# Performance work log

Hardware: AMD Instinct MI355X
Metric: run time of the kernel (lower is better)

## Reference

```python
import jax, jax.numpy as jnp
import numpy as np

N_NODES = 100000
N_EDGES = 600000
N_GRAPHS = 256
K = 5
N_FEAT = 16
N_CLASSES = 4


def setup_inputs() -> dict:
    key = jax.random.key(0)
    ks = jax.random.split(key, 12)
    x = jax.random.normal(ks[0], (N_NODES, N_FEAT), dtype=jnp.float32)
    edge_index = jax.random.randint(ks[1], (2, N_EDGES), 0, N_NODES, dtype=jnp.int32)
    batch = jnp.sort(jax.random.randint(ks[2], (N_NODES,), 0, N_GRAPHS, dtype=jnp.int32))
    s = 0.1
    W11 = jax.random.normal(ks[3], (K, N_FEAT, 64), dtype=jnp.float32) * s
    b11 = jnp.zeros((64,), dtype=jnp.float32)
    W12 = jax.random.normal(ks[4], (K, N_FEAT, 64), dtype=jnp.float32) * s
    b12 = jnp.zeros((64,), dtype=jnp.float32)
    W21 = jax.random.normal(ks[5], (K, 128, 256), dtype=jnp.float32) * s
    b21 = jnp.zeros((256,), dtype=jnp.float32)
    W22 = jax.random.normal(ks[6], (K, 128, 256), dtype=jnp.float32) * s
    b22 = jnp.zeros((256,), dtype=jnp.float32)
    fc_w = jax.random.normal(ks[7], (512, N_CLASSES), dtype=jnp.float32) * s
    fc_b = jnp.zeros((N_CLASSES,), dtype=jnp.float32)
    return {
        "x": x, "edge_index": edge_index, "batch": batch,
        "W11": W11, "b11": b11, "W12": W12, "b12": b12,
        "W21": W21, "b21": b21, "W22": W22, "b22": b22,
        "fc_w": fc_w, "fc_b": fc_b,
    }


def _cheb_norm(src, dst, n_nodes):
    # PyG ChebConv (sym norm, lambda_max=2): L_hat = -D^{-1/2} A D^{-1/2},
    # zero diagonal. Degree computed over source (row) indices.
    deg = jax.ops.segment_sum(jnp.ones_like(src, dtype=jnp.float32), src,
                              num_segments=n_nodes)
    dinv = jnp.where(deg > 0, jax.lax.rsqrt(jnp.maximum(deg, 1.0)), 0.0)
    return -dinv[src] * dinv[dst]


def _cheb_conv(x, src, dst, w_norm, W, b):
    # Chebyshev recursion: Tx0=x, Tx1=L_hat x, Txk = 2 L_hat Tx_{k-1} - Tx_{k-2}
    n = x.shape[0]

    def spmm(h):  # aggregate messages from src at dst
        return jax.ops.segment_sum(h[src] * w_norm[:, None], dst, num_segments=n)

    Tx0 = x
    Tx1 = spmm(x)
    out = jnp.einsum('nf,fo->no', Tx0, W[0]) + jnp.einsum('nf,fo->no', Tx1, W[1])
    for k in range(2, W.shape[0]):
        Tx2 = 2.0 * spmm(Tx1) - Tx0
        out = out + jnp.einsum('nf,fo->no', Tx2, W[k])
        Tx0, Tx1 = Tx1, Tx2
    return out + b


def reference(x, edge_index, batch, W11, b11, W12, b12, W21, b21, W22, b22,
              fc_w, fc_b):
    src, dst = edge_index[0], edge_index[1]
    w_fwd = _cheb_norm(src, dst, N_NODES)
    w_rev = _cheb_norm(dst, src, N_NODES)  # reversed adjacency

    x1 = jax.nn.relu(_cheb_conv(x, src, dst, w_fwd, W11, b11))
    x2 = jax.nn.relu(_cheb_conv(x, dst, src, w_rev, W12, b12))
    h = jnp.concatenate([x1, x2], axis=1)  # [N, 128]

    x1 = jax.nn.relu(_cheb_conv(h, src, dst, w_fwd, W21, b21))
    x2 = jax.nn.relu(_cheb_conv(h, dst, src, w_rev, W22, b22))
    h = jnp.concatenate([x1, x2], axis=1)  # [N, 512]

    # global mean pool over graphs
    sums = jax.ops.segment_sum(h, batch, num_segments=N_GRAPHS)
    cnt = jax.ops.segment_sum(jnp.ones((h.shape[0],), dtype=h.dtype), batch,
                              num_segments=N_GRAPHS)
    pooled = sums / jnp.maximum(cnt, 1.0)[:, None]  # [G, 512]

    logits = pooled @ fc_w + fc_b
    return jax.nn.log_softmax(logits, axis=1)
```

## Files before the change

### kernel.cpp

```cpp
#include <hip/hip_runtime.h>
#include <stdint.h>

#define NNODES 100000
#define NEDGES 600000
#define NGRAPH 256
#define KCH 5
#define F1 16
#define O1 64
#define F2 128
#define O2 256
#define FT1 (KCH * F1)
#define FT2 (KCH * F2)
#define KSTEPS 20
#define KS1 3
#define NBK 10
#define LROW2 72
#define NXCD 8

typedef unsigned short ushort_t;
typedef __attribute__((ext_vector_type(8))) short bf16x8;
typedef __attribute__((ext_vector_type(4))) float f32x4;

__device__ __forceinline__ float bflo(unsigned int u) {
    union { unsigned int u; float f; } v; v.u = u << 16; return v.f;
}
__device__ __forceinline__ float bfhi(unsigned int u) {
    union { unsigned int u; float f; } v; v.u = u & 0xFFFF0000u; return v.f;
}
__device__ __forceinline__ unsigned int f2bf(float f) {
    union { float f; unsigned int u; } v; v.f = f;
    return (v.u + 0x7FFFu + ((v.u >> 16) & 1u)) >> 16;
}
__device__ __forceinline__ unsigned int pack2(float lo, float hi) {
    return (f2bf(hi) << 16) | f2bf(lo);
}


__global__ void k_count(const int* __restrict__ src, const int* __restrict__ dst,
                        int* __restrict__ cntDst, int* __restrict__ cntSrc, int E) {
    int e = blockIdx.x * 256 + threadIdx.x;
    if (e < E) {
        atomicAdd(&cntDst[dst[e]], 1);
        atomicAdd(&cntSrc[src[e]], 1);
    }
}

__global__ void k_dinv(const int* __restrict__ cntDst, const int* __restrict__ cntSrc,
                       float* __restrict__ dinvF, float* __restrict__ dinvR, int n) {
    int i = blockIdx.x * 256 + threadIdx.x;
    if (i < n) {
        int cs = cntSrc[i], cd = cntDst[i];
        dinvF[i] = cs > 0 ? rsqrtf((float)cs) : 0.f;
        dinvR[i] = cd > 0 ? rsqrtf((float)cd) : 0.f;
    }
}

__global__ void k_scan1(const int* __restrict__ in, int* __restrict__ out,
                        int* __restrict__ blksum, int n) {
    __shared__ int a[512];
    __shared__ int s[256];
    int t = threadIdx.x;
    int base = blockIdx.x * 512;
    a[t]       = (base + t < n)       ? in[base + t]       : 0;
    a[t + 256] = (base + t + 256 < n) ? in[base + t + 256] : 0;
    __syncthreads();
    s[t] = a[2 * t] + a[2 * t + 1];
    __syncthreads();
    for (int off = 1; off < 256; off <<= 1) {
        int v = (t >= off) ? s[t - off] : 0;
        __syncthreads();
        s[t] += v;
        __syncthreads();
    }
    int ep = (t > 0) ? s[t - 1] : 0;
    if (base + 2 * t < n)     out[base + 2 * t]     = ep;
    if (base + 2 * t + 1 < n) out[base + 2 * t + 1] = ep + a[2 * t];
    if (t == 255) blksum[blockIdx.x] = s[255];
}

__global__ void k_scan2(int* __restrict__ blksum, int nb) {
    __shared__ int s[256];
    int t = threadIdx.x;
    s[t] = (t < nb) ? blksum[t] : 0;
    __syncthreads();
    for (int off = 1; off < 256; off <<= 1) {
        int v = (t >= off) ? s[t - off] : 0;
        __syncthreads();
        s[t] += v;
        __syncthreads();
    }
    if (t < nb) blksum[t] = (t > 0) ? s[t - 1] : 0;
}

__global__ void k_scan3(int* __restrict__ out, int* __restrict__ cur,
                        const int* __restrict__ blksum, int n) {
    int i = blockIdx.x * 512 + threadIdx.x;
    int add = blksum[blockIdx.x];
    if (i < n)       { int v = out[i] + add;       out[i] = v;       cur[i] = v; }
    if (i + 256 < n) { int v = out[i + 256] + add; out[i + 256] = v; cur[i + 256] = v; }
}

__global__ void k_tail(int* __restrict__ off_f, int* __restrict__ off_r, int n, int E) {
    if (threadIdx.x == 0) { off_f[n] = E; off_r[n] = E; }
}

__global__ void k_scatter(const int* __restrict__ src, const int* __restrict__ dst,
                          const float* __restrict__ dinvF, const float* __restrict__ dinvR,
                          int* __restrict__ curF, int* __restrict__ curR,
                          int2* __restrict__ edF, int2* __restrict__ edR, int E,
                          int chunk) {
    int c = blockIdx.x & (NXCD - 1);
    int sb = blockIdx.x >> 3;
    int slices = gridDim.x >> 3;
    int lo = c * chunk, hi = lo + chunk;
    for (int e = sb * 256 + threadIdx.x; e < E; e += slices * 256) {
        int s = src[e], d = dst[e];
        if (d >= lo && d < hi) {
            int p = atomicAdd(&curF[d], 1);
            float wf = -dinvF[s] * dinvF[d];
            edF[p] = make_int2(s, __float_as_int(wf));
        }
        if (s >= lo && s < hi) {
            int q = atomicAdd(&curR[s], 1);
            float wr = -dinvR[s] * dinvR[d];
            edR[q] = make_int2(d, __float_as_int(wr));
        }
    }
}

__global__ void k_gstart(const int* __restrict__ batch, int* __restrict__ gstart, int n) {
    int g = blockIdx.x * 64 + threadIdx.x;
    if (g > NGRAPH) return;
    if (g == NGRAPH) { gstart[g] = n; return; }
    int lo = 0, hi = n;
    while (lo < hi) {
        int mid = (lo + hi) >> 1;
        if (batch[mid] < g) lo = mid + 1; else hi = mid;
    }
    gstart[g] = lo;
}


__global__ void k_copyx(const float* __restrict__ x, float* __restrict__ Tx,
                        ushort_t* __restrict__ TxB, int n) {
    int tid = blockIdx.x * 256 + threadIdx.x;
    int r = tid >> 2, c = tid & 3;
    if (r < n) {
        float4 v = *(const float4*)(x + (size_t)r * 16 + c * 4);
        *(float4*)(Tx + (size_t)r * FT1 + c * 4) = v;
        uint2 b;
        b.x = pack2(v.x, v.y);
        b.y = pack2(v.z, v.w);
        *(uint2*)(TxB + (size_t)r * F1 + c * 4) = b;
    }
}

__global__ void k_spmm_f32(const ushort_t* __restrict__ HinB, float* __restrict__ Hout,
                           ushort_t* __restrict__ HoutB,
                           const float* __restrict__ Tx0,
                           const int* __restrict__ off, const int2* __restrict__ ed,
                           int n) {
    int tid = blockIdx.x * 256 + threadIdx.x;
    int r = tid >> 2, c = tid & 3;
    if (r >= n) return;
    int j0 = off[r], j1 = off[r + 1];
    float4 s = {0.f, 0.f, 0.f, 0.f};
    int j = j0;
    for (; j + 4 <= j1; j += 4) {
        int2 e0 = ed[j], e1 = ed[j + 1], e2 = ed[j + 2], e3 = ed[j + 3];
        float wa = __int_as_float(e0.y), wb = __int_as_float(e1.y);
        float wc = __int_as_float(e2.y), wd = __int_as_float(e3.y);
        const uint2 h0 = *(const uint2*)(HinB + (size_t)e0.x * F1 + c * 4);
        const uint2 h1 = *(const uint2*)(HinB + (size_t)e1.x * F1 + c * 4);
        const uint2 h2 = *(const uint2*)(HinB + (size_t)e2.x * F1 + c * 4);
        const uint2 h3 = *(const uint2*)(HinB + (size_t)e3.x * F1 + c * 4);
        s.x = fmaf(wa, bflo(h0.x), s.x); s.y = fmaf(wa, bfhi(h0.x), s.y);
        s.z = fmaf(wa, bflo(h0.y), s.z); s.w = fmaf(wa, bfhi(h0.y), s.w);
        s.x = fmaf(wb, bflo(h1.x), s.x); s.y = fmaf(wb, bfhi(h1.x), s.y);
        s.z = fmaf(wb, bflo(h1.y), s.z); s.w = fmaf(wb, bfhi(h1.y), s.w);
        s.x = fmaf(wc, bflo(h2.x), s.x); s.y = fmaf(wc, bfhi(h2.x), s.y);
        s.z = fmaf(wc, bflo(h2.y), s.z); s.w = fmaf(wc, bfhi(h2.y), s.w);
        s.x = fmaf(wd, bflo(h3.x), s.x); s.y = fmaf(wd, bfhi(h3.x), s.y);
        s.z = fmaf(wd, bflo(h3.y), s.z); s.w = fmaf(wd, bfhi(h3.y), s.w);
    }
    for (; j < j1; ++j) {
        int2 e = ed[j];
        float w2 = __int_as_float(e.y);
        const uint2 h = *(const uint2*)(HinB + (size_t)e.x * F1 + c * 4);
        s.x = fmaf(w2, bflo(h.x), s.x); s.y = fmaf(w2, bfhi(h.x), s.y);
        s.z = fmaf(w2, bflo(h.y), s.z); s.w = fmaf(w2, bfhi(h.y), s.w);
    }
    float4 o;
    if (Tx0) {
        const float4 t0 = *(const float4*)(Tx0 + (size_t)r * FT1 + c * 4);
        o.x = 2.f * s.x - t0.x; o.y = 2.f * s.y - t0.y;
        o.z = 2.f * s.z - t0.z; o.w = 2.f * s.w - t0.w;
    } else {
        o = s;
    }
    *(float4*)(Hout + (size_t)r * FT1 + c * 4) = o;
    uint2 b;
    b.x = pack2(o.x, o.y);
    b.y = pack2(o.z, o.w);
    *(uint2*)(HoutB + (size_t)r * F1 + c * 4) = b;
}

__global__ void k_spmm_bf(const ushort_t* __restrict__ Hin, ushort_t* __restrict__ Hout,
                          const ushort_t* __restrict__ Tx0,
                          const int* __restrict__ off, const int2* __restrict__ ed,
                          int n) {
    int r = blockIdx.x * 4 + (threadIdx.x >> 6);
    r = __builtin_amdgcn_readfirstlane(r);
    int c = threadIdx.x & 63;
    if (r >= n) return;
    int j0 = __builtin_amdgcn_readfirstlane(off[r]);
    int j1 = __builtin_amdgcn_readfirstlane(off[r + 1]);
    float s0 = 0.f, s1 = 0.f;
    int j = j0;
    int jfull = j0 + ((j1 - j0) & ~7);
    for (; j < jfull; j += 8) {
        float w[8];
        unsigned int h[8];
#pragma unroll
        for (int sl = 0; sl < 8; ++sl) {
            int2 e = ed[j + sl];
            w[sl] = __int_as_float(e.y);
            h[sl] = *(const unsigned int*)(Hin + (size_t)e.x * FT2 + c * 2);
        }
#pragma unroll
        for (int sl = 0; sl < 8; ++sl) {
            s0 = fmaf(bflo(h[sl]), w[sl], s0);
            s1 = fmaf(bfhi(h[sl]), w[sl], s1);
        }
    }
    int rem = j1 - j;
    if (rem) {
        float w[8];
        unsigned int h[8];
#pragma unroll
        for (int sl = 0; sl < 8; ++sl) {
            w[sl] = 0.f; h[sl] = 0u;
            if (sl < rem) {
                int2 e = ed[j + sl];
                w[sl] = __int_as_float(e.y);
                h[sl] = *(const unsigned int*)(Hin + (size_t)e.x * FT2 + c * 2);
            }
        }
#pragma unroll
        for (int sl = 0; sl < 8; ++sl) {
            s0 = fmaf(bflo(h[sl]), w[sl], s0);
            s1 = fmaf(bfhi(h[sl]), w[sl], s1);
        }
    }
    if (Tx0) {
        unsigned int t0 = *(const unsigned int*)(Tx0 + (size_t)r * FT2 + c * 2);
        s0 = 2.f * s0 - bflo(t0);
        s1 = 2.f * s1 - bfhi(t0);
    }
    *(unsigned int*)(Hout + (size_t)r * FT2 + c * 2) = pack2(s0, s1);
}

__global__ void k_packW1(const float* __restrict__ W, ushort_t* __restrict__ Bp) {
    int tid = blockIdx.x * 256 + threadIdx.x;
    if (tid >= 4 * KS1 * 64) return;
    int lane = tid & 63;
    int ks = (tid >> 6) % KS1;
    int nt = tid / (64 * KS1);
    int k0 = ks * 32 + (lane >> 4) * 8;
    int ncol = nt * 16 + (lane & 15);
    float v[8];
#pragma unroll
    for (int j = 0; j < 8; ++j) {
        int k = k0 + j;
        v[j] = (k < FT1) ? W[(size_t)k * O1 + ncol] : 0.f;
    }
    uint4 o;
    o.x = pack2(v[0], v[1]); o.y = pack2(v[2], v[3]);
    o.z = pack2(v[4], v[5]); o.w = pack2(v[6], v[7]);
    *(uint4*)(Bp + (size_t)tid * 8) = o;
}

__global__ __launch_bounds__(256) void k_gemm1_mfma(
    const float* __restrict__ A, const ushort_t* __restrict__ Bp,
    const float* __restrict__ bias, ushort_t* __restrict__ out, int n) {
    int lane = threadIdx.x & 63;
    int wvi = threadIdx.x >> 6;
    int mrow = lane & 15;
    int quad = lane >> 4;
    int m0w = blockIdx.x * 64 + wvi * 16;
    int row = m0w + mrow;
    int rowc = row < n ? row : n - 1;
    const float* Ar = A + (size_t)rowc * FT1 + quad * 8;

    f32x4 acc[4] = {};
#pragma unroll
    for (int ks = 0; ks < KS1; ++ks) {
        float4 a0 = *(const float4*)(Ar + ks * 32);
        float4 a1 = *(const float4*)(Ar + ks * 32 + 4);
        union { bf16x8 v; unsigned int u[4]; } ua;
        ua.u[0] = pack2(a0.x, a0.y);
        ua.u[1] = pack2(a0.z, a0.w);
        ua.u[2] = pack2(a1.x, a1.y);
        ua.u[3] = pack2(a1.z, a1.w);
#pragma unroll
        for (int nf = 0; nf < 4; ++nf) {
            bf16x8 bfr = *(const bf16x8*)(Bp + ((size_t)(nf * KS1 + ks) * 64 + lane) * 8);
            acc[nf] = __builtin_amdgcn_mfma_f32_16x16x32_bf16(ua.v, bfr, acc[nf], 0, 0, 0);
        }
    }
#pragma unroll
    for (int nf = 0; nf < 4; ++nf) {
        float bb = bias[nf * 16 + mrow];
#pragma unroll
        for (int reg = 0; reg < 4; ++reg) {
            int orow = m0w + quad * 4 + reg;
            if (orow < n)
                out[(size_t)orow * FT2 + nf * 16 + mrow] =
                    (ushort_t)f2bf(fmaxf(acc[nf][reg] + bb, 0.f));
        }
    }
}

__global__ void k_packW(const float* __restrict__ W, ushort_t* __restrict__ Bp) {
    int tid = blockIdx.x * 256 + threadIdx.x;
    if (tid >= 16 * KSTEPS * 64) return;
    int lane = tid & 63;
    int ks = (tid >> 6) % KSTEPS;
    int nt = tid / (64 * KSTEPS);
    int k0 = ks * 32 + (lane >> 4) * 8;
    int ncol = nt * 16 + (lane & 15);
    float v[8];
#pragma unroll
    for (int j = 0; j < 8; ++j) v[j] = W[(size_t)(k0 + j) * O2 + ncol];
    uint4 o;
    o.x = pack2(v[0], v[1]); o.y = pack2(v[2], v[3]);
    o.z = pack2(v[4], v[5]); o.w = pack2(v[6], v[7]);
    *(uint4*)(Bp + (size_t)tid * 8) = o;
}

__global__ __launch_bounds__(512) void k_gemm2_mfma(
    const ushort_t* __restrict__ A, const ushort_t* __restrict__ Bp,
    const float* __restrict__ bias, float* __restrict__ pooled, int colofs,
    const int* __restrict__ batch, int n) {
    __shared__ ushort_t lds[2][128 * LROW2];

    int lane = threadIdx.x & 63;
    int wv = threadIdx.x >> 6;
    int mhalf = wv >> 2;
    int nquad = wv & 3;
    int m0 = blockIdx.x * 128;
    int mrow = lane & 15;
    int quad = lane >> 4;
    int srow = threadIdx.x >> 2;
    int sc = threadIdx.x & 3;

    const ushort_t* Ag = A + (size_t)(m0 + srow) * FT2 + sc * 8;
    const ushort_t* Bbase = Bp + ((size_t)(nquad * 4) * KSTEPS * 64 + lane) * 8;
    int sidx = srow * LROW2 + sc * 8;
    int rbase = (mhalf * 64) * LROW2;

    f32x4 acc[4][4] = {};
    uint4 nxt0, nxt1;
    bf16x8 bcur[4], bnxt[4];

    *(uint4*)&lds[0][sidx]      = *(const uint4*)(Ag);
    *(uint4*)&lds[0][sidx + 32] = *(const uint4*)(Ag + 32);
    nxt0 = *(const uint4*)(Ag + 64);
    nxt1 = *(const uint4*)(Ag + 96);
#pragma unroll
    for (int nf = 0; nf < 4; ++nf)
        bcur[nf] = *(const bf16x8*)(Bbase + ((size_t)nf * KSTEPS) * 512);

    for (int bk = 0; bk < NBK; ++bk) {
        __syncthreads();
        if (bk + 1 < NBK) {
            *(uint4*)&lds[(bk + 1) & 1][sidx]      = nxt0;
            *(uint4*)&lds[(bk + 1) & 1][sidx + 32] = nxt1;
        }
        if (bk + 2 < NBK) {
            nxt0 = *(const uint4*)(Ag + (bk + 2) * 64);
            nxt1 = *(const uint4*)(Ag + (bk + 2) * 64 + 32);
        }
        const ushort_t* lbuf = &lds[bk & 1][0];
#pragma unroll
        for (int sub = 0; sub < 2; ++sub) {
            int ks = bk * 2 + sub;
            if (ks + 1 < KSTEPS) {
#pragma unroll
                for (int nf = 0; nf < 4; ++nf)
                    bnxt[nf] = *(const bf16x8*)(Bbase + ((size_t)nf * KSTEPS + ks + 1) * 512);
            }
            bf16x8 af[4];
#pragma unroll
            for (int mf = 0; mf < 4; ++mf)
                af[mf] = *(const bf16x8*)(lbuf + rbase + (mf * 16 + mrow) * LROW2 +
                                          sub * 32 + quad * 8);
#pragma unroll
            for (int mf = 0; mf < 4; ++mf)
#pragma unroll
                for (int nf = 0; nf < 4; ++nf)
                    acc[mf][nf] = __builtin_amdgcn_mfma_f32_16x16x32_bf16(
                        af[mf], bcur[nf], acc[mf][nf], 0, 0, 0);
#pragma unroll
            for (int nf = 0; nf < 4; ++nf) bcur[nf] = bnxt[nf];
        }
    }

    float bcol[4];
#pragma unroll
    for (int nf = 0; nf < 4; ++nf) bcol[nf] = bias[nquad * 64 + nf * 16 + mrow];

#pragma unroll
    for (int mf = 0; mf < 4; ++mf) {
        int t0 = m0 + mhalf * 64 + mf * 16;
        if (t0 >= n) break;
        int te = (t0 + 15 < n) ? t0 + 15 : n - 1;
        int r0 = t0 + quad * 4;
        if (batch[t0] == batch[te]) {
            int g = batch[t0];
#pragma unroll
            for (int nf = 0; nf < 4; ++nf) {
                float s = 0.f;
#pragma unroll
                for (int reg = 0; reg < 4; ++reg) {
                    float v = fmaxf(acc[mf][nf][reg] + bcol[nf], 0.f);
                    if (r0 + reg < n) s += v;
                }
                s += __shfl_xor(s, 16, 64);
                s += __shfl_xor(s, 32, 64);
                if (quad == 0)
                    atomicAdd(pooled + (size_t)g * 512 + colofs + nquad * 64 + nf * 16 + mrow, s);
            }
        } else {
            int gb[4];
#pragma unroll
            for (int reg = 0; reg < 4; ++reg)
                gb[reg] = batch[(r0 + reg < n) ? r0 + reg : n - 1];
#pragma unroll
            for (int nf = 0; nf < 4; ++nf) {
                int col = colofs + nquad * 64 + nf * 16 + mrow;
                float run = 0.f;
                int g = gb[0];
                bool any = false;
#pragma unroll
                for (int reg = 0; reg < 4; ++reg) {
                    int row = r0 + reg;
                    if (row >= n) break;
                    float v = fmaxf(acc[mf][nf][reg] + bcol[nf], 0.f);
                    if (gb[reg] != g) {
                        atomicAdd(pooled + (size_t)g * 512 + col, run);
                        run = 0.f;
                        g = gb[reg];
                    }
                    run += v;
                    any = true;
                }
                if (any) atomicAdd(pooled + (size_t)g * 512 + col, run);
            }
        }
    }
}

__global__ void k_logits(const float* __restrict__ pooled, const int* __restrict__ gstart,
                         const float* __restrict__ fcw, const float* __restrict__ fcb,
                         float* __restrict__ out) {
    int g = threadIdx.x;
    int cnt = gstart[g + 1] - gstart[g];
    float inv = 1.f / (float)(cnt > 1 ? cnt : 1);
    float lg[4];
#pragma unroll
    for (int o = 0; o < 4; ++o) lg[o] = fcb[o];
    for (int f = 0; f < 512; ++f) {
        float p = pooled[g * 512 + f] * inv;
#pragma unroll
        for (int o = 0; o < 4; ++o) lg[o] = fmaf(p, fcw[f * 4 + o], lg[o]);
    }
    float m = fmaxf(fmaxf(lg[0], lg[1]), fmaxf(lg[2], lg[3]));
    float s = 0.f;
#pragma unroll
    for (int o = 0; o < 4; ++o) s += expf(lg[o] - m);
    float l = logf(s);
#pragma unroll
    for (int o = 0; o < 4; ++o) out[g * 4 + o] = lg[o] - m - l;
}


extern "C" void kernel_launch(void* const* d_in, const int* in_sizes, int n_in,
                              void* d_out, int out_size, void* d_ws, size_t ws_size,
                              hipStream_t stream) {
    const float* x   = (const float*)d_in[0];
    const int* ei    = (const int*)d_in[1];
    const int* batch = (const int*)d_in[2];
    const float* W11 = (const float*)d_in[3];
    const float* b11 = (const float*)d_in[4];
    const float* W12 = (const float*)d_in[5];
    const float* b12 = (const float*)d_in[6];
    const float* W21 = (const float*)d_in[7];
    const float* b21 = (const float*)d_in[8];
    const float* W22 = (const float*)d_in[9];
    const float* b22 = (const float*)d_in[10];
    const float* fcw = (const float*)d_in[11];
    const float* fcb = (const float*)d_in[12];
    float* out = (float*)d_out;

    const int N = in_sizes[0] / F1;
    const int E = in_sizes[1] / 2;
    const int* src = ei;
    const int* dst = ei + E;

    char* w = (char*)d_ws;
    size_t pos = 0;
    auto alloc = [&](size_t bytes) -> void* {
        void* p = w + pos;
        pos += (bytes + 255) & ~(size_t)255;
        return p;
    };
    int* cur_f   = (int*)alloc((size_t)N * 4);
    int* cur_r   = (int*)alloc((size_t)N * 4);
    int* off_f   = (int*)alloc((size_t)(N + 1) * 4);
    int* off_r   = (int*)alloc((size_t)(N + 1) * 4);
    float* dinvF = (float*)alloc((size_t)N * 4);
    float* dinvR = (float*)alloc((size_t)N * 4);
    int2* ed_f   = (int2*)alloc((size_t)E * 8);
    int2* ed_r   = (int2*)alloc((size_t)E * 8);
    int* blks_f  = (int*)alloc(1024);
    int* blks_r  = (int*)alloc(1024);
    int* gstart  = (int*)alloc((NGRAPH + 1) * 4);
    float* pooled = (float*)alloc((size_t)NGRAPH * 512 * 4);
    ushort_t* BpF = (ushort_t*)alloc((size_t)FT2 * O2 * 2);
    ushort_t* BpR = (ushort_t*)alloc((size_t)FT2 * O2 * 2);
    ushort_t* Bp1F = (ushort_t*)alloc((size_t)4 * KS1 * 64 * 8 * 2);
    ushort_t* Bp1R = (ushort_t*)alloc((size_t)4 * KS1 * 64 * 8 * 2);
    float* TxAll1 = (float*)alloc(((size_t)N * FT1 + 256) * 4);
    ushort_t* TxB1 = (ushort_t*)alloc((size_t)KCH * N * F1 * 2);
    ushort_t* TxAll2 = (ushort_t*)alloc((size_t)(N + 128) * FT2 * 2);

    (void)hipMemsetAsync(cur_f, 0, (size_t)N * 4, stream);
    (void)hipMemsetAsync(cur_r, 0, (size_t)N * 4, stream);
    (void)hipMemsetAsync(pooled, 0, (size_t)NGRAPH * 512 * 4, stream);

    int gE = (E + 255) / 256, gN = (N + 255) / 256;
    k_count<<<gE, 256, 0, stream>>>(src, dst, cur_f, cur_r, E);
    k_dinv<<<gN, 256, 0, stream>>>(cur_f, cur_r, dinvF, dinvR, N);

    int NB = (N + 511) / 512;
    k_scan1<<<NB, 256, 0, stream>>>(cur_f, off_f, blks_f, N);
    k_scan1<<<NB, 256, 0, stream>>>(cur_r, off_r, blks_r, N);
    k_scan2<<<1, 256, 0, stream>>>(blks_f, NB);
    k_scan2<<<1, 256, 0, stream>>>(blks_r, NB);
    k_scan3<<<NB, 256, 0, stream>>>(off_f, cur_f, blks_f, N);
    k_scan3<<<NB, 256, 0, stream>>>(off_r, cur_r, blks_r, N);
    k_tail<<<1, 64, 0, stream>>>(off_f, off_r, N, E);
    int chunk = (N + NXCD - 1) / NXCD;
    k_scatter<<<NXCD * 256, 256, 0, stream>>>(src, dst, dinvF, dinvR, cur_f, cur_r,
                                              ed_f, ed_r, E, chunk);
    k_gstart<<<5, 64, 0, stream>>>(batch, gstart, N);
    k_packW<<<80, 256, 0, stream>>>(W21, BpF);
    k_packW<<<80, 256, 0, stream>>>(W22, BpR);
    k_packW1<<<3, 256, 0, stream>>>(W11, Bp1F);
    k_packW1<<<3, 256, 0, stream>>>(W12, Bp1R);

    k_copyx<<<(N * 4 + 255) / 256, 256, 0, stream>>>(x, TxAll1, TxB1, N);
    int gs1 = (N * 4 + 255) / 256;
    int gg1 = (N + 63) / 64;
    auto C1 = [&](int k) { return TxAll1 + k * F1; };
    auto B1 = [&](int k) { return TxB1 + (size_t)k * N * F1; };
    k_spmm_f32<<<gs1, 256, 0, stream>>>(B1(0), C1(1), B1(1), nullptr, off_f, ed_f, N);
    k_spmm_f32<<<gs1, 256, 0, stream>>>(B1(1), C1(2), B1(2), C1(0), off_f, ed_f, N);
    k_spmm_f32<<<gs1, 256, 0, stream>>>(B1(2), C1(3), B1(3), C1(1), off_f, ed_f, N);
    k_spmm_f32<<<gs1, 256, 0, stream>>>(B1(3), C1(4), B1(4), C1(2), off_f, ed_f, N);
    k_gemm1_mfma<<<gg1, 256, 0, stream>>>(TxAll1, Bp1F, b11, TxAll2, N);
    k_spmm_f32<<<gs1, 256, 0, stream>>>(B1(0), C1(1), B1(1), nullptr, off_r, ed_r, N);
    k_spmm_f32<<<gs1, 256, 0, stream>>>(B1(1), C1(2), B1(2), C1(0), off_r, ed_r, N);
    k_spmm_f32<<<gs1, 256, 0, stream>>>(B1(2), C1(3), B1(3), C1(1), off_r, ed_r, N);
    k_spmm_f32<<<gs1, 256, 0, stream>>>(B1(3), C1(4), B1(4), C1(2), off_r, ed_r, N);
    k_gemm1_mfma<<<gg1, 256, 0, stream>>>(TxAll1, Bp1R, b12, TxAll2 + O1, N);

    int gs2 = (N + 3) / 4;
    auto C2 = [&](int k) { return TxAll2 + k * F2; };
    int gg = (N + 127) / 128;
    k_spmm_bf<<<gs2, 256, 0, stream>>>(C2(0), C2(1), nullptr, off_f, ed_f, N);
    k_spmm_bf<<<gs2, 256, 0, stream>>>(C2(1), C2(2), C2(0), off_f, ed_f, N);
    k_spmm_bf<<<gs2, 256, 0, stream>>>(C2(2), C2(3), C2(1), off_f, ed_f, N);
    k_spmm_bf<<<gs2, 256, 0, stream>>>(C2(3), C2(4), C2(2), off_f, ed_f, N);
    k_gemm2_mfma<<<gg, 512, 0, stream>>>(TxAll2, BpF, b21, pooled, 0, batch, N);
    k_spmm_bf<<<gs2, 256, 0, stream>>>(C2(0), C2(1), nullptr, off_r, ed_r, N);
    k_spmm_bf<<<gs2, 256, 0, stream>>>(C2(1), C2(2), C2(0), off_r, ed_r, N);
    k_spmm_bf<<<gs2, 256, 0, stream>>>(C2(2), C2(3), C2(1), off_r, ed_r, N);
    k_spmm_bf<<<gs2, 256, 0, stream>>>(C2(3), C2(4), C2(2), off_r, ed_r, N);
    k_gemm2_mfma<<<gg, 512, 0, stream>>>(TxAll2, BpR, b22, pooled, 256, batch, N);

    k_logits<<<1, 256, 0, stream>>>(pooled, gstart, fcw, fcb, out);
}
```

Baseline: 794.2 us.

## Merge setup kernels, software-pipeline bf16 SpMM, retile layer-2 GEMM to 4 waves

Several independent changes land together. The forward and reverse scan and weight-pack kernels are merged into single launches, and the tail write is folded into the scan, which cuts launch count. The last layer-1 SpMM step no longer writes an unused bf16 copy. The bf16 SpMM gets a two-block double-buffered gather so that loads of the next 8 edges overlap the FMAs on the current ones. The layer-2 MFMA GEMM moves from 8 waves with 64-wide K blocks to 4 waves with 128 rows per wave and 32-wide K steps, which raises per-wave register use and relies on launch_bounds(256,2) for occupancy.

```diff
diff --git a/kernel.cpp b/kernel.cpp
--- a/kernel.cpp
+++ b/kernel.cpp
@@ -13,8 +13,7 @@
 #define FT2 (KCH * F2)
 #define KSTEPS 20
 #define KS1 3
-#define NBK 10
-#define LROW2 72
+#define LROW 40
 #define NXCD 8
 
 typedef unsigned short ushort_t;
@@ -55,12 +54,18 @@
     }
 }
 
-__global__ void k_scan1(const int* __restrict__ in, int* __restrict__ out,
-                        int* __restrict__ blksum, int n) {
+__global__ void k_scan1m(const int* __restrict__ inF, int* __restrict__ outF,
+                         int* __restrict__ bsF,
+                         const int* __restrict__ inR, int* __restrict__ outR,
+                         int* __restrict__ bsR, int n, int NB) {
     __shared__ int a[512];
     __shared__ int s[256];
+    int b = blockIdx.x;
+    const int* in; int* out; int* bs; int lb;
+    if (b < NB) { in = inF; out = outF; bs = bsF; lb = b; }
+    else        { in = inR; out = outR; bs = bsR; lb = b - NB; }
     int t = threadIdx.x;
-    int base = blockIdx.x * 512;
+    int base = lb * 512;
     a[t]       = (base + t < n)       ? in[base + t]       : 0;
     a[t + 256] = (base + t + 256 < n) ? in[base + t + 256] : 0;
     __syncthreads();
@@ -75,13 +80,14 @@
     int ep = (t > 0) ? s[t - 1] : 0;
     if (base + 2 * t < n)     out[base + 2 * t]     = ep;
     if (base + 2 * t + 1 < n) out[base + 2 * t + 1] = ep + a[2 * t];
-    if (t == 255) blksum[blockIdx.x] = s[255];
-}
-
-__global__ void k_scan2(int* __restrict__ blksum, int nb) {
+    if (t == 255) bs[lb] = s[255];
+}
+
+__global__ void k_scan2m(int* __restrict__ bsF, int* __restrict__ bsR, int nb) {
     __shared__ int s[256];
+    int* bs = (blockIdx.x == 0) ? bsF : bsR;
     int t = threadIdx.x;
-    s[t] = (t < nb) ? blksum[t] : 0;
+    s[t] = (t < nb) ? bs[t] : 0;
     __syncthreads();
     for (int off = 1; off < 256; off <<= 1) {
         int v = (t >= off) ? s[t - off] : 0;
@@ -89,19 +95,22 @@
         s[t] += v;
         __syncthreads();
     }
-    if (t < nb) blksum[t] = (t > 0) ? s[t - 1] : 0;
-}
-
-__global__ void k_scan3(int* __restrict__ out, int* __restrict__ cur,
-                        const int* __restrict__ blksum, int n) {
-    int i = blockIdx.x * 512 + threadIdx.x;
-    int add = blksum[blockIdx.x];
+    if (t < nb) bs[t] = (t > 0) ? s[t - 1] : 0;
+}
+
+__global__ void k_scan3m(int* __restrict__ outF, int* __restrict__ curF,
+                         const int* __restrict__ bsF,
+                         int* __restrict__ outR, int* __restrict__ curR,
+                         const int* __restrict__ bsR, int n, int E, int NB) {
+    int b = blockIdx.x;
+    int* out; int* cur; const int* bs; int lb;
+    if (b < NB) { out = outF; cur = curF; bs = bsF; lb = b; }
+    else        { out = outR; cur = curR; bs = bsR; lb = b - NB; }
+    int i = lb * 512 + threadIdx.x;
+    int add = bs[lb];
     if (i < n)       { int v = out[i] + add;       out[i] = v;       cur[i] = v; }
     if (i + 256 < n) { int v = out[i + 256] + add; out[i + 256] = v; cur[i + 256] = v; }
-}
-
-__global__ void k_tail(int* __restrict__ off_f, int* __restrict__ off_r, int n, int E) {
-    if (threadIdx.x == 0) { off_f[n] = E; off_r[n] = E; }
+    if (lb == 0 && threadIdx.x == 0) out[n] = E;
 }
 
 __global__ void k_scatter(const int* __restrict__ src, const int* __restrict__ dst,
@@ -199,10 +208,12 @@
         o = s;
     }
     *(float4*)(Hout + (size_t)r * FT1 + c * 4) = o;
-    uint2 b;
-    b.x = pack2(o.x, o.y);
-    b.y = pack2(o.z, o.w);
-    *(uint2*)(HoutB + (size_t)r * F1 + c * 4) = b;
+    if (HoutB) {
+        uint2 b;
+        b.x = pack2(o.x, o.y);
+        b.y = pack2(o.z, o.w);
+        *(uint2*)(HoutB + (size_t)r * F1 + c * 4) = b;
+    }
 }
 
 __global__ void k_spmm_bf(const ushort_t* __restrict__ Hin, ushort_t* __restrict__ Hout,
@@ -216,40 +227,47 @@
     int j0 = __builtin_amdgcn_readfirstlane(off[r]);
     int j1 = __builtin_amdgcn_readfirstlane(off[r + 1]);
     float s0 = 0.f, s1 = 0.f;
-    int j = j0;
-    int jfull = j0 + ((j1 - j0) & ~7);
-    for (; j < jfull; j += 8) {
-        float w[8];
-        unsigned int h[8];
+
+    auto loadblk = [&](int jb, float* W, unsigned int* H) {
+        if (jb + 8 <= j1) {
+#pragma unroll
+            for (int sl = 0; sl < 8; ++sl) {
+                int2 e = ed[jb + sl];
+                W[sl] = __int_as_float(e.y);
+                H[sl] = *(const unsigned int*)(Hin + (size_t)e.x * FT2 + c * 2);
+            }
+        } else {
+#pragma unroll
+            for (int sl = 0; sl < 8; ++sl) {
+                W[sl] = 0.f; H[sl] = 0u;
+                if (jb + sl < j1) {
+                    int2 e = ed[jb + sl];
+                    W[sl] = __int_as_float(e.y);
+                    H[sl] = *(const unsigned int*)(Hin + (size_t)e.x * FT2 + c * 2);
+                }
+            }
+        }
+    };
+    auto fmablk = [&](const float* W, const unsigned int* H) {
 #pragma unroll
         for (int sl = 0; sl < 8; ++sl) {
-            int2 e = ed[j + sl];
-            w[sl] = __int_as_float(e.y);
-            h[sl] = *(const unsigned int*)(Hin + (size_t)e.x * FT2 + c * 2);
-        }
-#pragma unroll
-        for (int sl = 0; sl < 8; ++sl) {
-            s0 = fmaf(bflo(h[sl]), w[sl], s0);
-            s1 = fmaf(bfhi(h[sl]), w[sl], s1);
-        }
-    }
-    int rem = j1 - j;
-    if (rem) {
-        float w[8];
-        unsigned int h[8];
-#pragma unroll
-        for (int sl = 0; sl < 8; ++sl) {
-            w[sl] = 0.f; h[sl] = 0u;
-            if (sl < rem) {
-                int2 e = ed[j + sl];
-                w[sl] = __int_as_float(e.y);
-                h[sl] = *(const unsigned int*)(Hin + (size_t)e.x * FT2 + c * 2);
+            s0 = fmaf(bflo(H[sl]), W[sl], s0);
+            s1 = fmaf(bfhi(H[sl]), W[sl], s1);
+        }
+    };
+
+    float wA[8], wB[8];
+    unsigned int hA[8], hB[8];
+    if (j0 < j1) {
+        loadblk(j0, wA, hA);
+        for (int j = j0; j < j1; j += 16) {
+            bool hasB = (j + 8 < j1);
+            if (hasB) loadblk(j + 8, wB, hB);
+            fmablk(wA, hA);
+            if (hasB) {
+                if (j + 16 < j1) loadblk(j + 16, wA, hA);
+                fmablk(wB, hB);
             }
-        }
-#pragma unroll
-        for (int sl = 0; sl < 8; ++sl) {
-            s0 = fmaf(bflo(h[sl]), w[sl], s0);
-            s1 = fmaf(bfhi(h[sl]), w[sl], s1);
         }
     }
     if (Tx0) {
@@ -260,8 +278,12 @@
     *(unsigned int*)(Hout + (size_t)r * FT2 + c * 2) = pack2(s0, s1);
 }
 
-__global__ void k_packW1(const float* __restrict__ W, ushort_t* __restrict__ Bp) {
-    int tid = blockIdx.x * 256 + threadIdx.x;
+__global__ void k_packW1m(const float* __restrict__ WF, ushort_t* __restrict__ BpF_,
+                          const float* __restrict__ WR, ushort_t* __restrict__ BpR_) {
+    int b = blockIdx.x;
+    const float* W = (b < 3) ? WF : WR;
+    ushort_t* Bp = (b < 3) ? BpF_ : BpR_;
+    int tid = ((b < 3) ? b : b - 3) * 256 + threadIdx.x;
     if (tid >= 4 * KS1 * 64) return;
     int lane = tid & 63;
     int ks = (tid >> 6) % KS1;
@@ -321,8 +343,12 @@
     }
 }
 
-__global__ void k_packW(const float* __restrict__ W, ushort_t* __restrict__ Bp) {
-    int tid = blockIdx.x * 256 + threadIdx.x;
+__global__ void k_packWm(const float* __restrict__ WF, ushort_t* __restrict__ BpF_,
+                         const float* __restrict__ WR, ushort_t* __restrict__ BpR_) {
+    int b = blockIdx.x;
+    const float* W = (b < 80) ? WF : WR;
+    ushort_t* Bp = (b < 80) ? BpF_ : BpR_;
+    int tid = ((b < 80) ? b : b - 80) * 256 + threadIdx.x;
     if (tid >= 16 * KSTEPS * 64) return;
     int lane = tid & 63;
     int ks = (tid >> 6) % KSTEPS;
@@ -338,81 +364,73 @@
     *(uint4*)(Bp + (size_t)tid * 8) = o;
 }
 
-__global__ __launch_bounds__(512) void k_gemm2_mfma(
+__global__ __launch_bounds__(256, 2) void k_gemm2_mfma(
     const ushort_t* __restrict__ A, const ushort_t* __restrict__ Bp,
     const float* __restrict__ bias, float* __restrict__ pooled, int colofs,
     const int* __restrict__ batch, int n) {
-    __shared__ ushort_t lds[2][128 * LROW2];
+    __shared__ ushort_t lds[2][128 * LROW];
 
     int lane = threadIdx.x & 63;
     int wv = threadIdx.x >> 6;
-    int mhalf = wv >> 2;
-    int nquad = wv & 3;
     int m0 = blockIdx.x * 128;
     int mrow = lane & 15;
     int quad = lane >> 4;
-    int srow = threadIdx.x >> 2;
-    int sc = threadIdx.x & 3;
-
-    const ushort_t* Ag = A + (size_t)(m0 + srow) * FT2 + sc * 8;
-    const ushort_t* Bbase = Bp + ((size_t)(nquad * 4) * KSTEPS * 64 + lane) * 8;
-    int sidx = srow * LROW2 + sc * 8;
-    int rbase = (mhalf * 64) * LROW2;
-
-    f32x4 acc[4][4] = {};
+    int srow = threadIdx.x >> 1;
+    int sc = threadIdx.x & 1;
+
+    const ushort_t* Ag = A + (size_t)(m0 + srow) * FT2 + sc * 16;
+    const ushort_t* Bbase = Bp + ((size_t)(wv * 4) * KSTEPS * 64 + lane) * 8;
+    int sidx = srow * LROW + sc * 16;
+
+    f32x4 acc[8][4] = {};
     uint4 nxt0, nxt1;
     bf16x8 bcur[4], bnxt[4];
 
-    *(uint4*)&lds[0][sidx]      = *(const uint4*)(Ag);
-    *(uint4*)&lds[0][sidx + 32] = *(const uint4*)(Ag + 32);
-    nxt0 = *(const uint4*)(Ag + 64);
-    nxt1 = *(const uint4*)(Ag + 96);
+    *(uint4*)&lds[0][sidx]     = *(const uint4*)(Ag);
+    *(uint4*)&lds[0][sidx + 8] = *(const uint4*)(Ag + 8);
+    nxt0 = *(const uint4*)(Ag + 32);
+    nxt1 = *(const uint4*)(Ag + 40);
 #pragma unroll
     for (int nf = 0; nf < 4; ++nf)
         bcur[nf] = *(const bf16x8*)(Bbase + ((size_t)nf * KSTEPS) * 512);
 
-    for (int bk = 0; bk < NBK; ++bk) {
+    for (int ks = 0; ks < KSTEPS; ++ks) {
         __syncthreads();
-        if (bk + 1 < NBK) {
-            *(uint4*)&lds[(bk + 1) & 1][sidx]      = nxt0;
-            *(uint4*)&lds[(bk + 1) & 1][sidx + 32] = nxt1;
-        }
-        if (bk + 2 < NBK) {
-            nxt0 = *(const uint4*)(Ag + (bk + 2) * 64);
-            nxt1 = *(const uint4*)(Ag + (bk + 2) * 64 + 32);
-        }
-        const ushort_t* lbuf = &lds[bk & 1][0];
-#pragma unroll
-        for (int sub = 0; sub < 2; ++sub) {
-            int ks = bk * 2 + sub;
-            if (ks + 1 < KSTEPS) {
-#pragma unroll
-                for (int nf = 0; nf < 4; ++nf)
-                    bnxt[nf] = *(const bf16x8*)(Bbase + ((size_t)nf * KSTEPS + ks + 1) * 512);
-            }
-            bf16x8 af[4];
-#pragma unroll
-            for (int mf = 0; mf < 4; ++mf)
-                af[mf] = *(const bf16x8*)(lbuf + rbase + (mf * 16 + mrow) * LROW2 +
-                                          sub * 32 + quad * 8);
-#pragma unroll
-            for (int mf = 0; mf < 4; ++mf)
-#pragma unroll
-                for (int nf = 0; nf < 4; ++nf)
-                    acc[mf][nf] = __builtin_amdgcn_mfma_f32_16x16x32_bf16(
-                        af[mf], bcur[nf], acc[mf][nf], 0, 0, 0);
-#pragma unroll
-            for (int nf = 0; nf < 4; ++nf) bcur[nf] = bnxt[nf];
-        }
+        if (ks + 1 < KSTEPS) {
+            *(uint4*)&lds[(ks + 1) & 1][sidx]     = nxt0;
+            *(uint4*)&lds[(ks + 1) & 1][sidx + 8] = nxt1;
+        }
+        if (ks + 2 < KSTEPS) {
+            nxt0 = *(const uint4*)(Ag + (ks + 2) * 32);
+            nxt1 = *(const uint4*)(Ag + (ks + 2) * 32 + 8);
+        }
+        if (ks + 1 < KSTEPS) {
+#pragma unroll
+            for (int nf = 0; nf < 4; ++nf)
+                bnxt[nf] = *(const bf16x8*)(Bbase + ((size_t)nf * KSTEPS + ks + 1) * 512);
+        }
+        const ushort_t* lbuf = &lds[ks & 1][0];
+        bf16x8 af[8];
+#pragma unroll
+        for (int mf = 0; mf < 8; ++mf)
+            af[mf] = *(const bf16x8*)(lbuf + (mf * 16 + mrow) * LROW + quad * 8);
+#pragma unroll
+        for (int mf = 0; mf < 8; ++mf)
+#pragma unroll
+            for (int nf = 0; nf < 4; ++nf)
+                acc[mf][nf] = __builtin_amdgcn_mfma_f32_16x16x32_bf16(
+                    af[mf], bcur[nf], acc[mf][nf], 0, 0, 0);
+#pragma unroll
+        for (int nf = 0; nf < 4; ++nf) bcur[nf] = bnxt[nf];
     }
 
     float bcol[4];
 #pragma unroll
-    for (int nf = 0; nf < 4; ++nf) bcol[nf] = bias[nquad * 64 + nf * 16 + mrow];
-
-#pragma unroll
-    for (int mf = 0; mf < 4; ++mf) {
-        int t0 = m0 + mhalf * 64 + mf * 16;
+    for (int nf = 0; nf < 4; ++nf) bcol[nf] = bias[wv * 64 + nf * 16 + mrow];
+
+#pragma unroll
+    for (int mf = 0; mf < 8; ++mf) {
+        int t0 = m0 + mf * 16;
         if (t0 >= n) break;
         int te = (t0 + 15 < n) ? t0 + 15 : n - 1;
         int r0 = t0 + quad * 4;
@@ -429,7 +447,7 @@
                 s += __shfl_xor(s, 16, 64);
                 s += __shfl_xor(s, 32, 64);
                 if (quad == 0)
-                    atomicAdd(pooled + (size_t)g * 512 + colofs + nquad * 64 + nf * 16 + mrow, s);
+                    atomicAdd(pooled + (size_t)g * 512 + colofs + wv * 64 + nf * 16 + mrow, s);
             }
         } else {
             int gb[4];
@@ -438,7 +456,7 @@
                 gb[reg] = batch[(r0 + reg < n) ? r0 + reg : n - 1];
 #pragma unroll
             for (int nf = 0; nf < 4; ++nf) {
-                int col = colofs + nquad * 64 + nf * 16 + mrow;
+                int col = colofs + wv * 64 + nf * 16 + mrow;
                 float run = 0.f;
                 int g = gb[0];
                 bool any = false;
@@ -544,21 +562,15 @@
     k_dinv<<<gN, 256, 0, stream>>>(cur_f, cur_r, dinvF, dinvR, N);
 
     int NB = (N + 511) / 512;
-    k_scan1<<<NB, 256, 0, stream>>>(cur_f, off_f, blks_f, N);
-    k_scan1<<<NB, 256, 0, stream>>>(cur_r, off_r, blks_r, N);
-    k_scan2<<<1, 256, 0, stream>>>(blks_f, NB);
-    k_scan2<<<1, 256, 0, stream>>>(blks_r, NB);
-    k_scan3<<<NB, 256, 0, stream>>>(off_f, cur_f, blks_f, N);
-    k_scan3<<<NB, 256, 0, stream>>>(off_r, cur_r, blks_r, N);
-    k_tail<<<1, 64, 0, stream>>>(off_f, off_r, N, E);
+    k_scan1m<<<2 * NB, 256, 0, stream>>>(cur_f, off_f, blks_f, cur_r, off_r, blks_r, N, NB);
+    k_scan2m<<<2, 256, 0, stream>>>(blks_f, blks_r, NB);
+    k_scan3m<<<2 * NB, 256, 0, stream>>>(off_f, cur_f, blks_f, off_r, cur_r, blks_r, N, E, NB);
     int chunk = (N + NXCD - 1) / NXCD;
     k_scatter<<<NXCD * 256, 256, 0, stream>>>(src, dst, dinvF, dinvR, cur_f, cur_r,
                                               ed_f, ed_r, E, chunk);
     k_gstart<<<5, 64, 0, stream>>>(batch, gstart, N);
-    k_packW<<<80, 256, 0, stream>>>(W21, BpF);
-    k_packW<<<80, 256, 0, stream>>>(W22, BpR);
-    k_packW1<<<3, 256, 0, stream>>>(W11, Bp1F);
-    k_packW1<<<3, 256, 0, stream>>>(W12, Bp1R);
+    k_packWm<<<160, 256, 0, stream>>>(W21, BpF, W22, BpR);
+    k_packW1m<<<6, 256, 0, stream>>>(W11, Bp1F, W12, Bp1R);
 
     k_copyx<<<(N * 4 + 255) / 256, 256, 0, stream>>>(x, TxAll1, TxB1, N);
     int gs1 = (N * 4 + 255) / 256;
@@ -568,12 +580,12 @@
     k_spmm_f32<<<gs1, 256, 0, stream>>>(B1(0), C1(1), B1(1), nullptr, off_f, ed_f, N);
     k_spmm_f32<<<gs1, 256, 0, stream>>>(B1(1), C1(2), B1(2), C1(0), off_f, ed_f, N);
     k_spmm_f32<<<gs1, 256, 0, stream>>>(B1(2), C1(3), B1(3), C1(1), off_f, ed_f, N);
-    k_spmm_f32<<<gs1, 256, 0, stream>>>(B1(3), C1(4), B1(4), C1(2), off_f, ed_f, N);
+    k_spmm_f32<<<gs1, 256, 0, stream>>>(B1(3), C1(4), nullptr, C1(2), off_f, ed_f, N);
     k_gemm1_mfma<<<gg1, 256, 0, stream>>>(TxAll1, Bp1F, b11, TxAll2, N);
     k_spmm_f32<<<gs1, 256, 0, stream>>>(B1(0), C1(1), B1(1), nullptr, off_r, ed_r, N);
     k_spmm_f32<<<gs1, 256, 0, stream>>>(B1(1), C1(2), B1(2), C1(0), off_r, ed_r, N);
     k_spmm_f32<<<gs1, 256, 0, stream>>>(B1(2), C1(3), B1(3), C1(1), off_r, ed_r, N);
-    k_spmm_f32<<<gs1, 256, 0, stream>>>(B1(3), C1(4), B1(4), C1(2), off_r, ed_r, N);
+    k_spmm_f32<<<gs1, 256, 0, stream>>>(B1(3), C1(4), nullptr, C1(2), off_r, ed_r, N);
     k_gemm1_mfma<<<gg1, 256, 0, stream>>>(TxAll1, Bp1R, b12, TxAll2 + O1, N);
 
     int gs2 = (N + 3) / 4;
@@ -583,12 +595,12 @@
     k_spmm_bf<<<gs2, 256, 0, stream>>>(C2(1), C2(2), C2(0), off_f, ed_f, N);
     k_spmm_bf<<<gs2, 256, 0, stream>>>(C2(2), C2(3), C2(1), off_f, ed_f, N);
     k_spmm_bf<<<gs2, 256, 0, stream>>>(C2(3), C2(4), C2(2), off_f, ed_f, N);
-    k_gemm2_mfma<<<gg, 512, 0, stream>>>(TxAll2, BpF, b21, pooled, 0, batch, N);
+    k_gemm2_mfma<<<gg, 256, 0, stream>>>(TxAll2, BpF, b21, pooled, 0, batch, N);
     k_spmm_bf<<<gs2, 256, 0, stream>>>(C2(0), C2(1), nullptr, off_r, ed_r, N);
     k_spmm_bf<<<gs2, 256, 0, stream>>>(C2(1), C2(2), C2(0), off_r, ed_r, N);
     k_spmm_bf<<<gs2, 256, 0, stream>>>(C2(2), C2(3), C2(1), off_r, ed_r, N);
     k_spmm_bf<<<gs2, 256, 0, stream>>>(C2(3), C2(4), C2(2), off_r, ed_r, N);
-    k_gemm2_mfma<<<gg, 512, 0, stream>>>(TxAll2, BpR, b22, pooled, 256, batch, N);
+    k_gemm2_mfma<<<gg, 256, 0, stream>>>(TxAll2, BpR, b22, pooled, 256, batch, N);
 
     k_logits<<<1, 256, 0, stream>>>(pooled, gstart, fcw, fcb, out);
 }
```

Result: no change. 792.3 us (-0.3%).
